# Kernel tuning notes

Hardware: AMD Instinct MI355X
Metric: run time of the kernel (lower is better)

## Reference

```python
import jax, jax.numpy as jnp
import numpy as np

B, H, L, D = 2, 16, 2048, 64

def _linear_feature_map(x, W):
    # x: [B,H,L,D], W: [H,D,E] -> relu(x @ W) per head, [B,H,L,E]
    return jax.nn.relu(jnp.einsum('bhld,hde->bhle', x, W))

def setup_inputs() -> dict:
    key = jax.random.key(0)
    ks = jax.random.split(key, 5)
    return {
        'query_states': jax.random.normal(ks[0], (B, H, L, D), dtype=jnp.float32),
        'key_states':   jax.random.normal(ks[1], (B, H, L, D), dtype=jnp.float32),
        'value_states': jax.random.normal(ks[2], (B, H, L, D), dtype=jnp.float32),
        'fm_q_weight':  jax.random.normal(ks[3], (H, D, D), dtype=jnp.float32),
        'fm_k_weight':  jax.random.normal(ks[4], (H, D, D), dtype=jnp.float32),
    }

def reference(query_states, key_states, value_states, fm_q_weight, fm_k_weight):
    # NOTE: source applies feature_map_k to queries and feature_map_q to keys (swapped); keep faithful.
    fq = _linear_feature_map(query_states, fm_k_weight)  # [B,H,L,D]
    fk = _linear_feature_map(key_states, fm_q_weight)    # [B,H,L,D]
    attn = jnp.einsum('bhld,bhkd->bhlk', fq, fk)         # [B,H,L,L]
    attn = jnp.tril(attn)                                # causal mask (attention_mask=None path)
    attn = attn / jnp.sum(attn, axis=-1, keepdims=True)  # row-normalize
    out = jnp.einsum('bhlk,bhkd->bhld', attn, value_states)
    return (out, attn)
```

## Files before the change

kernel.cpp:

```cpp
#include <hip/hip_runtime.h>
#include <hip/hip_bf16.h>

#define BB 2
#define HH 16
#define LL 2048
#define DD 64
constexpr int BH = BB * HH;
constexpr int NT = LL / 64;

typedef __attribute__((ext_vector_type(8))) short bf16x8;
typedef __attribute__((ext_vector_type(4))) float f32x4;

typedef unsigned short u16;
typedef unsigned int u32;

__device__ __forceinline__ u16 f2bf(float x) {
    __bf16 b = (__bf16)x;
    u16 u; __builtin_memcpy(&u, &b, 2);
    return u;
}
__device__ __forceinline__ float bf2f(u16 u) {
    union { u32 i; float f; } c; c.i = ((u32)u) << 16; return c.f;
}

__device__ __forceinline__ void gll16(const void* gptr, void* ldsptr) {
    __builtin_amdgcn_global_load_lds(
        (const u32 __attribute__((address_space(1)))*)gptr,
        (u32 __attribute__((address_space(3)))*)ldsptr, 16, 0, 0);
}

__device__ __forceinline__ bf16x8 ld_frag(const char* tile, int row, int kbyte) {
    return *(const bf16x8*)(tile + row * 128 + (kbyte ^ ((row & 7) << 4)));
}

template<bool TSUM>
__global__ __launch_bounds__(256) void fmap2_kernel(
    const float* __restrict__ x, const float* __restrict__ W,
    u16* __restrict__ ghi, float* __restrict__ tsum)
{
    __shared__ float sXT[64][64];
    __shared__ float sW[64][64];
    int bx = blockIdx.x;
    int bh = bx / NT, rb = bx % NT;
    int h = bh % HH;
    const float* xp = x + (size_t)bh * LL * DD + (size_t)rb * 64 * DD;
    const float* wp = W + (size_t)h * DD * DD;

    int tid = threadIdx.x;
    {
        int r = tid >> 2, c0 = (tid & 3) * 16;
        for (int u = 0; u < 16; u += 4) {
            float4 t = *(const float4*)(xp + r * DD + c0 + u);
            sXT[c0 + u + 0][r] = t.x; sXT[c0 + u + 1][r] = t.y;
            sXT[c0 + u + 2][r] = t.z; sXT[c0 + u + 3][r] = t.w;
            *(float4*)(&sW[r][c0 + u]) = *(const float4*)(wp + r * DD + c0 + u);
        }
    }
    __syncthreads();

    int ty = tid >> 4, tx = tid & 15;
    float acc[4][4] = {};
    #pragma unroll 4
    for (int d = 0; d < 64; ++d) {
        float4 a = *(const float4*)(&sXT[d][ty * 4]);
        float4 b = *(const float4*)(&sW[d][tx * 4]);
        float av[4] = {a.x, a.y, a.z, a.w};
        float bv[4] = {b.x, b.y, b.z, b.w};
        #pragma unroll
        for (int j = 0; j < 4; ++j)
            #pragma unroll
            for (int i = 0; i < 4; ++i)
                acc[j][i] = fmaf(av[j], bv[i], acc[j][i]);
    }

    char* hib = (char*)ghi + (size_t)bx * 8192;
    float colsum[4] = {0.f, 0.f, 0.f, 0.f};
    #pragma unroll
    for (int j = 0; j < 4; ++j) {
        int rr = ty * 4 + j;
        ushort4 hv;
        hv.x = f2bf(fmaxf(acc[j][0], 0.f));
        hv.y = f2bf(fmaxf(acc[j][1], 0.f));
        hv.z = f2bf(fmaxf(acc[j][2], 0.f));
        hv.w = f2bf(fmaxf(acc[j][3], 0.f));
        int off = rr * 128 + ((tx * 8) ^ ((rr & 7) << 4));
        *(ushort4*)(hib + off) = hv;
        if constexpr (TSUM) {
            colsum[0] += bf2f(hv.x); colsum[1] += bf2f(hv.y);
            colsum[2] += bf2f(hv.z); colsum[3] += bf2f(hv.w);
        }
    }

    if constexpr (TSUM) {
        __syncthreads();
        #pragma unroll
        for (int i = 0; i < 4; ++i)
            sXT[ty][tx * 4 + i] = colsum[i];
        __syncthreads();
        if (tid < 64) {
            float s = 0.f;
            #pragma unroll
            for (int y = 0; y < 16; ++y) s += sXT[y][tid];
            tsum[(size_t)bx * 64 + tid] = s;
        }
    }
}

__global__ __launch_bounds__(256) void vprep_kernel(
    const float* __restrict__ v, u16* __restrict__ vt)
{
    int bx = blockIdx.x;
    int bh = bx >> 5, ct = bx & 31;
    int t = threadIdx.x;
    int c0 = (t >> 4) * 4, e0 = (t & 15) * 4;
    const float* vp = v + ((size_t)bh * LL + (size_t)ct * 64) * DD;

    float ld[4][4];
    #pragma unroll
    for (int j = 0; j < 4; ++j) {
        float4 f = *(const float4*)(vp + (size_t)(c0 + j) * DD + e0);
        ld[j][0] = f.x; ld[j][1] = f.y; ld[j][2] = f.z; ld[j][3] = f.w;
    }
    char* base = (char*)vt + (size_t)bx * 8192;
    #pragma unroll
    for (int i = 0; i < 4; ++i) {
        int e = e0 + i;
        ushort4 wv;
        wv.x = f2bf(ld[0][i]); wv.y = f2bf(ld[1][i]);
        wv.z = f2bf(ld[2][i]); wv.w = f2bf(ld[3][i]);
        *(ushort4*)(base + e * 128 + ((c0 * 2) ^ ((e & 7) << 4))) = wv;
    }
}

__global__ __launch_bounds__(64) void tprefix_kernel(
    const float* __restrict__ tsum, float* __restrict__ pex)
{
    int bh = blockIdx.x, d = threadIdx.x;
    float run = 0.f;
    for (int t = 0; t < NT; ++t) {
        size_t i = ((size_t)bh * NT + t) * 64 + d;
        pex[i] = run;
        run += tsum[i];
    }
}

__global__ __launch_bounds__(256) void rowsum_kernel(
    const u16* __restrict__ khi, const u16* __restrict__ qhi,
    const float* __restrict__ pex, float* __restrict__ rinv)
{
    __shared__ float wsum[4][64];
    int bx = blockIdx.x;
    int bh = bx >> 5, t = bx & 31;
    int w = threadIdx.x >> 6, d = threadIdx.x & 63;
    const size_t tb = ((size_t)bh * NT + t) * 4096;

    float fkv[16];
    float s = 0.f;
    #pragma unroll
    for (int i = 0; i < 16; ++i) {
        int r = w * 16 + i;
        size_t idx = tb + r * 64 + (d ^ ((r & 7) << 3));
        fkv[i] = bf2f(khi[idx]);
        s += fkv[i];
    }
    wsum[w][d] = s;
    __syncthreads();

    float cs = pex[((size_t)bh * NT + t) * 64 + d];
    for (int w2 = 0; w2 < w; ++w2) cs += wsum[w2][d];

    #pragma unroll
    for (int i = 0; i < 16; ++i) {
        int r = w * 16 + i;
        size_t idx = tb + r * 64 + (d ^ ((r & 7) << 3));
        cs += fkv[i];
        float tt = bf2f(qhi[idx]) * cs;
        #pragma unroll
        for (int o = 1; o < 64; o <<= 1) tt += __shfl_xor(tt, o);
        if (d == 0) rinv[(size_t)bh * LL + t * 64 + r] = 1.0f / tt;
    }
}

__global__ __launch_bounds__(256, 4) void attn4_kernel(
    const u16* __restrict__ qhi, const u16* __restrict__ khi,
    const u16* __restrict__ vt, const float* __restrict__ rinvg,
    float* __restrict__ outO, float* __restrict__ outA)
{
    __shared__ __align__(16) char lds[40960];
    char* sS = lds + 32768;

    int bx = blockIdx.x;
    int bh = (bx & 7) * 4 + (bx >> 8);
    int jj = (bx >> 3) & 31;
    int rblk = (jj & 1) ? (jj >> 1) : (31 - (jj >> 1));
    int brow = rblk * 64;

    int tid = threadIdx.x;
    int w = tid >> 6, l = tid & 63;
    int l15 = l & 15, lq = l >> 4;
    int o = tid * 16, wb = w << 10;

    {
        const char* qT = (const char*)qhi + ((size_t)bh * NT + rblk) * 8192;
        gll16(qT + o,        lds + 16384 + wb);
        gll16(qT + o + 4096, lds + 16384 + wb + 4096);

        const char* kT = (const char*)khi + (size_t)bh * NT * 8192;
        const char* vT = (const char*)vt  + (size_t)bh * NT * 8192;
        gll16(kT + o,        lds + wb);
        gll16(kT + o + 4096, lds + wb + 4096);
        gll16(vT + o,        lds + 8192 + wb);
        gll16(vT + o + 4096, lds + 8192 + wb + 4096);
    }
    float ri = rinvg[(size_t)bh * LL + brow + w * 16 + l15];
    asm volatile("s_waitcnt vmcnt(0)" ::: "memory");
    __syncthreads();

    int qrow = w * 16 + l15;
    bf16x8 bq[2];
    #pragma unroll
    for (int ks = 0; ks < 2; ++ks)
        bq[ks] = ld_frag(lds + 16384, qrow, lq * 16 + ks * 64);
    __syncthreads();

    f32x4 acc2[4];
    #pragma unroll
    for (int eb = 0; eb < 4; ++eb) acc2[eb] = (f32x4){0.f, 0.f, 0.f, 0.f};

    for (int ct = 0; ct <= rblk; ++ct) {
        char* cur = lds + (ct & 1) * 16384;

        if (ct < rblk) {
            char* nxt = lds + ((ct + 1) & 1) * 16384;
            const char* kT = (const char*)khi + ((size_t)bh * NT + ct + 1) * 8192;
            const char* vT = (const char*)vt  + ((size_t)bh * NT + ct + 1) * 8192;
            gll16(kT + o,        nxt + wb);
            gll16(kT + o + 4096, nxt + wb + 4096);
            gll16(vT + o,        nxt + 8192 + wb);
            gll16(vT + o + 4096, nxt + 8192 + wb + 4096);
        }

        f32x4 sa[4];
        #pragma unroll
        for (int cb = 0; cb < 4; ++cb) sa[cb] = (f32x4){0.f, 0.f, 0.f, 0.f};
        #pragma unroll
        for (int ks = 0; ks < 2; ++ks) {
            #pragma unroll
            for (int cb = 0; cb < 4; ++cb) {
                bf16x8 ah = ld_frag(cur, cb * 16 + l15, lq * 16 + ks * 64);
                sa[cb] = __builtin_amdgcn_mfma_f32_16x16x32_bf16(ah, bq[ks], sa[cb], 0, 0, 0);
            }
        }

        bool diag = (ct == rblk);
        int srow = w * 16 + l15;
        #pragma unroll
        for (int cb = 0; cb < 4; ++cb) {
            if (diag) {
                #pragma unroll
                for (int rg = 0; rg < 4; ++rg)
                    if (cb * 16 + lq * 4 + rg > srow) sa[cb][rg] = 0.f;
            }
            sa[cb] *= ri;
            ushort4 pv;
            pv.x = f2bf(sa[cb][0]); pv.y = f2bf(sa[cb][1]);
            pv.z = f2bf(sa[cb][2]); pv.w = f2bf(sa[cb][3]);
            int soff = srow * 128 + ((cb * 32 + lq * 8) ^ ((srow & 7) << 4));
            *(ushort4*)(sS + soff) = pv;
        }

        asm volatile("s_waitcnt lgkmcnt(0)" ::: "memory");
        __builtin_amdgcn_sched_barrier(0);
        __builtin_amdgcn_s_barrier();
        __builtin_amdgcn_sched_barrier(0);

        {
            int bcol = ct * 64;
            float* atile = outA + ((size_t)bh * LL + brow) * LL + bcol;
            #pragma unroll
            for (int u = 0; u < 4; ++u) {
                int idx = tid + u * 256;
                int r = idx >> 4;
                int c = idx & 15;
                ushort4 pv = *(const ushort4*)(sS + r * 128 + ((c * 8) ^ ((r & 7) << 4)));
                f32x4 o4 = { bf2f(pv.x), bf2f(pv.y), bf2f(pv.z), bf2f(pv.w) };
                __builtin_nontemporal_store(o4, (f32x4*)(atile + (size_t)r * LL + c * 4));
            }
        }

        bf16x8 pf[2];
        #pragma unroll
        for (int ks = 0; ks < 2; ++ks)
            pf[ks] = ld_frag(sS, srow, lq * 16 + ks * 64);
        #pragma unroll
        for (int ks = 0; ks < 2; ++ks) {
            #pragma unroll
            for (int eb = 0; eb < 4; ++eb) {
                bf16x8 av = ld_frag(cur + 8192, eb * 16 + l15, lq * 16 + ks * 64);
                acc2[eb] = __builtin_amdgcn_mfma_f32_16x16x32_bf16(av, pf[ks], acc2[eb], 0, 0, 0);
            }
        }

        __syncthreads();
    }

    f32x4 z = {0.f, 0.f, 0.f, 0.f};
    for (int ct2 = rblk + 1; ct2 < NT; ++ct2) {
        int bcol = ct2 * 64;
        #pragma unroll
        for (int u = 0; u < 4; ++u) {
            int idx = tid + u * 256;
            int r = idx >> 4, c4 = idx & 15;
            __builtin_nontemporal_store(z,
                (f32x4*)(outA + ((size_t)bh * LL + brow + r) * LL + bcol + c4 * 4));
        }
    }

    float* oo = outO + ((size_t)bh * LL + brow + w * 16 + l15) * DD;
    #pragma unroll
    for (int eb = 0; eb < 4; ++eb) {
        float4 o4 = { acc2[eb][0], acc2[eb][1], acc2[eb][2], acc2[eb][3] };
        *(float4*)(oo + eb * 16 + lq * 4) = o4;
    }
}

extern "C" void kernel_launch(void* const* d_in, const int* in_sizes, int n_in,
                              void* d_out, int out_size, void* d_ws, size_t ws_size,
                              hipStream_t stream)
{
    (void)in_sizes; (void)n_in; (void)out_size; (void)ws_size;
    const float* q  = (const float*)d_in[0];
    const float* k  = (const float*)d_in[1];
    const float* v  = (const float*)d_in[2];
    const float* Wq = (const float*)d_in[3];
    const float* Wk = (const float*)d_in[4];

    float* out  = (float*)d_out;
    float* attn = out + (size_t)BB * HH * LL * DD;

    const size_t TILE_HW = (size_t)BH * NT * 4096;
    u16* QHI = (u16*)d_ws;
    u16* KHI = QHI + TILE_HW;
    u16* VT  = KHI + TILE_HW;
    float* RINV = (float*)(VT + TILE_HW);
    float* TSUM = RINV + (size_t)BH * LL;
    float* PEX  = TSUM + (size_t)BH * NT * 64;

    fmap2_kernel<false><<<BH * NT, 256, 0, stream>>>(q, Wk, QHI, nullptr);
    fmap2_kernel<true><<<BH * NT, 256, 0, stream>>>(k, Wq, KHI, TSUM);
    vprep_kernel<<<BH * NT, 256, 0, stream>>>(v, VT);
    tprefix_kernel<<<BH, 64, 0, stream>>>(TSUM, PEX);
    rowsum_kernel<<<BH * NT, 256, 0, stream>>>(KHI, QHI, PEX, RINV);
    attn4_kernel<<<BH * NT, 256, 0, stream>>>(QHI, KHI, VT, RINV, out, attn);
}
```

Measured before the change: 173.0 us.

## Fuse V prep and tile prefix into other kernels; pair row blocks per attention block

Measured after the change: 175.1 us. No clear change (+1.2%).

```diff
diff --git a/kernel.cpp b/kernel.cpp
--- a/kernel.cpp
+++ b/kernel.cpp
@@ -33,10 +33,11 @@
     return *(const bf16x8*)(tile + row * 128 + (kbyte ^ ((row & 7) << 4)));
 }
 
-template<bool TSUM>
+template<bool TSUM, bool VPREP>
 __global__ __launch_bounds__(256) void fmap2_kernel(
     const float* __restrict__ x, const float* __restrict__ W,
-    u16* __restrict__ ghi, float* __restrict__ tsum)
+    u16* __restrict__ ghi, float* __restrict__ tsum,
+    const float* __restrict__ v, u16* __restrict__ vt)
 {
     __shared__ float sXT[64][64];
     __shared__ float sW[64][64];
@@ -104,49 +105,31 @@
             tsum[(size_t)bx * 64 + tid] = s;
         }
     }
-}
-
-__global__ __launch_bounds__(256) void vprep_kernel(
-    const float* __restrict__ v, u16* __restrict__ vt)
-{
-    int bx = blockIdx.x;
-    int bh = bx >> 5, ct = bx & 31;
-    int t = threadIdx.x;
-    int c0 = (t >> 4) * 4, e0 = (t & 15) * 4;
-    const float* vp = v + ((size_t)bh * LL + (size_t)ct * 64) * DD;
-
-    float ld[4][4];
-    #pragma unroll
-    for (int j = 0; j < 4; ++j) {
-        float4 f = *(const float4*)(vp + (size_t)(c0 + j) * DD + e0);
-        ld[j][0] = f.x; ld[j][1] = f.y; ld[j][2] = f.z; ld[j][3] = f.w;
-    }
-    char* base = (char*)vt + (size_t)bx * 8192;
-    #pragma unroll
-    for (int i = 0; i < 4; ++i) {
-        int e = e0 + i;
-        ushort4 wv;
-        wv.x = f2bf(ld[0][i]); wv.y = f2bf(ld[1][i]);
-        wv.z = f2bf(ld[2][i]); wv.w = f2bf(ld[3][i]);
-        *(ushort4*)(base + e * 128 + ((c0 * 2) ^ ((e & 7) << 4))) = wv;
-    }
-}
-
-__global__ __launch_bounds__(64) void tprefix_kernel(
-    const float* __restrict__ tsum, float* __restrict__ pex)
-{
-    int bh = blockIdx.x, d = threadIdx.x;
-    float run = 0.f;
-    for (int t = 0; t < NT; ++t) {
-        size_t i = ((size_t)bh * NT + t) * 64 + d;
-        pex[i] = run;
-        run += tsum[i];
+
+    if constexpr (VPREP) {
+        int c0 = (tid >> 4) * 4, e0 = (tid & 15) * 4;
+        const float* vp = v + ((size_t)bh * LL + (size_t)rb * 64) * DD;
+        float ld[4][4];
+        #pragma unroll
+        for (int j = 0; j < 4; ++j) {
+            float4 f = *(const float4*)(vp + (size_t)(c0 + j) * DD + e0);
+            ld[j][0] = f.x; ld[j][1] = f.y; ld[j][2] = f.z; ld[j][3] = f.w;
+        }
+        char* base = (char*)vt + (size_t)bx * 8192;
+        #pragma unroll
+        for (int i = 0; i < 4; ++i) {
+            int e = e0 + i;
+            ushort4 wv;
+            wv.x = f2bf(ld[0][i]); wv.y = f2bf(ld[1][i]);
+            wv.z = f2bf(ld[2][i]); wv.w = f2bf(ld[3][i]);
+            *(ushort4*)(base + e * 128 + ((c0 * 2) ^ ((e & 7) << 4))) = wv;
+        }
     }
 }
 
 __global__ __launch_bounds__(256) void rowsum_kernel(
     const u16* __restrict__ khi, const u16* __restrict__ qhi,
-    const float* __restrict__ pex, float* __restrict__ rinv)
+    const float* __restrict__ tsum, float* __restrict__ rinv)
 {
     __shared__ float wsum[4][64];
     int bx = blockIdx.x;
@@ -166,7 +149,9 @@
     wsum[w][d] = s;
     __syncthreads();
 
-    float cs = pex[((size_t)bh * NT + t) * 64 + d];
+    float cs = 0.f;
+    for (int t2 = 0; t2 < t; ++t2)
+        cs += tsum[((size_t)bh * NT + t2) * 64 + d];
     for (int w2 = 0; w2 < w; ++w2) cs += wsum[w2][d];
 
     #pragma unroll
@@ -181,7 +166,7 @@
     }
 }
 
-__global__ __launch_bounds__(256, 4) void attn4_kernel(
+__global__ __launch_bounds__(256, 4) void attn5_kernel(
     const u16* __restrict__ qhi, const u16* __restrict__ khi,
     const u16* __restrict__ vt, const float* __restrict__ rinvg,
     float* __restrict__ outO, float* __restrict__ outA)
@@ -190,137 +175,140 @@
     char* sS = lds + 32768;
 
     int bx = blockIdx.x;
-    int bh = (bx & 7) * 4 + (bx >> 8);
-    int jj = (bx >> 3) & 31;
-    int rblk = (jj & 1) ? (jj >> 1) : (31 - (jj >> 1));
-    int brow = rblk * 64;
+    int bh = bx & 31;
+    int p = bx >> 5;
 
     int tid = threadIdx.x;
     int w = tid >> 6, l = tid & 63;
     int l15 = l & 15, lq = l >> 4;
     int o = tid * 16, wb = w << 10;
 
-    {
-        const char* qT = (const char*)qhi + ((size_t)bh * NT + rblk) * 8192;
-        gll16(qT + o,        lds + 16384 + wb);
-        gll16(qT + o + 4096, lds + 16384 + wb + 4096);
-
-        const char* kT = (const char*)khi + (size_t)bh * NT * 8192;
-        const char* vT = (const char*)vt  + (size_t)bh * NT * 8192;
-        gll16(kT + o,        lds + wb);
-        gll16(kT + o + 4096, lds + wb + 4096);
-        gll16(vT + o,        lds + 8192 + wb);
-        gll16(vT + o + 4096, lds + 8192 + wb + 4096);
-    }
-    float ri = rinvg[(size_t)bh * LL + brow + w * 16 + l15];
-    asm volatile("s_waitcnt vmcnt(0)" ::: "memory");
-    __syncthreads();
-
-    int qrow = w * 16 + l15;
-    bf16x8 bq[2];
-    #pragma unroll
-    for (int ks = 0; ks < 2; ++ks)
-        bq[ks] = ld_frag(lds + 16384, qrow, lq * 16 + ks * 64);
-    __syncthreads();
-
-    f32x4 acc2[4];
-    #pragma unroll
-    for (int eb = 0; eb < 4; ++eb) acc2[eb] = (f32x4){0.f, 0.f, 0.f, 0.f};
-
-    for (int ct = 0; ct <= rblk; ++ct) {
-        char* cur = lds + (ct & 1) * 16384;
-
-        if (ct < rblk) {
-            char* nxt = lds + ((ct + 1) & 1) * 16384;
-            const char* kT = (const char*)khi + ((size_t)bh * NT + ct + 1) * 8192;
-            const char* vT = (const char*)vt  + ((size_t)bh * NT + ct + 1) * 8192;
-            gll16(kT + o,        nxt + wb);
-            gll16(kT + o + 4096, nxt + wb + 4096);
-            gll16(vT + o,        nxt + 8192 + wb);
-            gll16(vT + o + 4096, nxt + 8192 + wb + 4096);
-        }
-
-        f32x4 sa[4];
-        #pragma unroll
-        for (int cb = 0; cb < 4; ++cb) sa[cb] = (f32x4){0.f, 0.f, 0.f, 0.f};
-        #pragma unroll
-        for (int ks = 0; ks < 2; ++ks) {
+    for (int half = 0; half < 2; ++half) {
+        int rblk = half ? (31 - p) : p;
+        int brow = rblk * 64;
+
+        {
+            const char* qT = (const char*)qhi + ((size_t)bh * NT + rblk) * 8192;
+            gll16(qT + o,        lds + 16384 + wb);
+            gll16(qT + o + 4096, lds + 16384 + wb + 4096);
+
+            const char* kT = (const char*)khi + (size_t)bh * NT * 8192;
+            const char* vT = (const char*)vt  + (size_t)bh * NT * 8192;
+            gll16(kT + o,        lds + wb);
+            gll16(kT + o + 4096, lds + wb + 4096);
+            gll16(vT + o,        lds + 8192 + wb);
+            gll16(vT + o + 4096, lds + 8192 + wb + 4096);
+        }
+        float ri = rinvg[(size_t)bh * LL + brow + w * 16 + l15];
+        asm volatile("s_waitcnt vmcnt(0)" ::: "memory");
+        __syncthreads();
+
+        int qrow = w * 16 + l15;
+        bf16x8 bq[2];
+        #pragma unroll
+        for (int ks = 0; ks < 2; ++ks)
+            bq[ks] = ld_frag(lds + 16384, qrow, lq * 16 + ks * 64);
+        __syncthreads();
+
+        f32x4 acc2[4];
+        #pragma unroll
+        for (int eb = 0; eb < 4; ++eb) acc2[eb] = (f32x4){0.f, 0.f, 0.f, 0.f};
+
+        for (int ct = 0; ct <= rblk; ++ct) {
+            char* cur = lds + (ct & 1) * 16384;
+
+            if (ct < rblk) {
+                char* nxt = lds + ((ct + 1) & 1) * 16384;
+                const char* kT = (const char*)khi + ((size_t)bh * NT + ct + 1) * 8192;
+                const char* vT = (const char*)vt  + ((size_t)bh * NT + ct + 1) * 8192;
+                gll16(kT + o,        nxt + wb);
+                gll16(kT + o + 4096, nxt + wb + 4096);
+                gll16(vT + o,        nxt + 8192 + wb);
+                gll16(vT + o + 4096, nxt + 8192 + wb + 4096);
+            }
+
+            f32x4 sa[4];
+            #pragma unroll
+            for (int cb = 0; cb < 4; ++cb) sa[cb] = (f32x4){0.f, 0.f, 0.f, 0.f};
+            #pragma unroll
+            for (int ks = 0; ks < 2; ++ks) {
+                #pragma unroll
+                for (int cb = 0; cb < 4; ++cb) {
+                    bf16x8 ah = ld_frag(cur, cb * 16 + l15, lq * 16 + ks * 64);
+                    sa[cb] = __builtin_amdgcn_mfma_f32_16x16x32_bf16(ah, bq[ks], sa[cb], 0, 0, 0);
+                }
+            }
+
+            bool diag = (ct == rblk);
+            int srow = w * 16 + l15;
             #pragma unroll
             for (int cb = 0; cb < 4; ++cb) {
-                bf16x8 ah = ld_frag(cur, cb * 16 + l15, lq * 16 + ks * 64);
-                sa[cb] = __builtin_amdgcn_mfma_f32_16x16x32_bf16(ah, bq[ks], sa[cb], 0, 0, 0);
-            }
-        }
-
-        bool diag = (ct == rblk);
-        int srow = w * 16 + l15;
-        #pragma unroll
-        for (int cb = 0; cb < 4; ++cb) {
-            if (diag) {
+                if (diag) {
+                    #pragma unroll
+                    for (int rg = 0; rg < 4; ++rg)
+                        if (cb * 16 + lq * 4 + rg > srow) sa[cb][rg] = 0.f;
+                }
+                sa[cb] *= ri;
+                ushort4 pv;
+                pv.x = f2bf(sa[cb][0]); pv.y = f2bf(sa[cb][1]);
+                pv.z = f2bf(sa[cb][2]); pv.w = f2bf(sa[cb][3]);
+                int soff = srow * 128 + ((cb * 32 + lq * 8) ^ ((srow & 7) << 4));
+                *(ushort4*)(sS + soff) = pv;
+            }
+
+            asm volatile("s_waitcnt lgkmcnt(0)" ::: "memory");
+            __builtin_amdgcn_sched_barrier(0);
+            __builtin_amdgcn_s_barrier();
+            __builtin_amdgcn_sched_barrier(0);
+
+            {
+                int bcol = ct * 64;
+                float* atile = outA + ((size_t)bh * LL + brow) * LL + bcol;
                 #pragma unroll
-                for (int rg = 0; rg < 4; ++rg)
-                    if (cb * 16 + lq * 4 + rg > srow) sa[cb][rg] = 0.f;
-            }
-            sa[cb] *= ri;
-            ushort4 pv;
-            pv.x = f2bf(sa[cb][0]); pv.y = f2bf(sa[cb][1]);
-            pv.z = f2bf(sa[cb][2]); pv.w = f2bf(sa[cb][3]);
-            int soff = srow * 128 + ((cb * 32 + lq * 8) ^ ((srow & 7) << 4));
-            *(ushort4*)(sS + soff) = pv;
-        }
-
-        asm volatile("s_waitcnt lgkmcnt(0)" ::: "memory");
-        __builtin_amdgcn_sched_barrier(0);
-        __builtin_amdgcn_s_barrier();
-        __builtin_amdgcn_sched_barrier(0);
-
-        {
-            int bcol = ct * 64;
-            float* atile = outA + ((size_t)bh * LL + brow) * LL + bcol;
+                for (int u = 0; u < 4; ++u) {
+                    int idx = tid + u * 256;
+                    int r = idx >> 4;
+                    int c = idx & 15;
+                    ushort4 pv = *(const ushort4*)(sS + r * 128 + ((c * 8) ^ ((r & 7) << 4)));
+                    f32x4 o4 = { bf2f(pv.x), bf2f(pv.y), bf2f(pv.z), bf2f(pv.w) };
+                    __builtin_nontemporal_store(o4, (f32x4*)(atile + (size_t)r * LL + c * 4));
+                }
+            }
+
+            bf16x8 pf[2];
+            #pragma unroll
+            for (int ks = 0; ks < 2; ++ks)
+                pf[ks] = ld_frag(sS, srow, lq * 16 + ks * 64);
+            #pragma unroll
+            for (int ks = 0; ks < 2; ++ks) {
+                #pragma unroll
+                for (int eb = 0; eb < 4; ++eb) {
+                    bf16x8 av = ld_frag(cur + 8192, eb * 16 + l15, lq * 16 + ks * 64);
+                    acc2[eb] = __builtin_amdgcn_mfma_f32_16x16x32_bf16(av, pf[ks], acc2[eb], 0, 0, 0);
+                }
+            }
+
+            __syncthreads();
+        }
+
+        f32x4 z = {0.f, 0.f, 0.f, 0.f};
+        for (int ct2 = rblk + 1; ct2 < NT; ++ct2) {
+            int bcol = ct2 * 64;
             #pragma unroll
             for (int u = 0; u < 4; ++u) {
                 int idx = tid + u * 256;
-                int r = idx >> 4;
-                int c = idx & 15;
-                ushort4 pv = *(const ushort4*)(sS + r * 128 + ((c * 8) ^ ((r & 7) << 4)));
-                f32x4 o4 = { bf2f(pv.x), bf2f(pv.y), bf2f(pv.z), bf2f(pv.w) };
-                __builtin_nontemporal_store(o4, (f32x4*)(atile + (size_t)r * LL + c * 4));
-            }
-        }
-
-        bf16x8 pf[2];
-        #pragma unroll
-        for (int ks = 0; ks < 2; ++ks)
-            pf[ks] = ld_frag(sS, srow, lq * 16 + ks * 64);
-        #pragma unroll
-        for (int ks = 0; ks < 2; ++ks) {
-            #pragma unroll
-            for (int eb = 0; eb < 4; ++eb) {
-                bf16x8 av = ld_frag(cur + 8192, eb * 16 + l15, lq * 16 + ks * 64);
-                acc2[eb] = __builtin_amdgcn_mfma_f32_16x16x32_bf16(av, pf[ks], acc2[eb], 0, 0, 0);
-            }
-        }
-
-        __syncthreads();
-    }
-
-    f32x4 z = {0.f, 0.f, 0.f, 0.f};
-    for (int ct2 = rblk + 1; ct2 < NT; ++ct2) {
-        int bcol = ct2 * 64;
-        #pragma unroll
-        for (int u = 0; u < 4; ++u) {
-            int idx = tid + u * 256;
-            int r = idx >> 4, c4 = idx & 15;
-            __builtin_nontemporal_store(z,
-                (f32x4*)(outA + ((size_t)bh * LL + brow + r) * LL + bcol + c4 * 4));
-        }
-    }
-
-    float* oo = outO + ((size_t)bh * LL + brow + w * 16 + l15) * DD;
-    #pragma unroll
-    for (int eb = 0; eb < 4; ++eb) {
-        float4 o4 = { acc2[eb][0], acc2[eb][1], acc2[eb][2], acc2[eb][3] };
-        *(float4*)(oo + eb * 16 + lq * 4) = o4;
+                int r = idx >> 4, c4 = idx & 15;
+                __builtin_nontemporal_store(z,
+                    (f32x4*)(outA + ((size_t)bh * LL + brow + r) * LL + bcol + c4 * 4));
+            }
+        }
+
+        float* oo = outO + ((size_t)bh * LL + brow + w * 16 + l15) * DD;
+        #pragma unroll
+        for (int eb = 0; eb < 4; ++eb) {
+            float4 o4 = { acc2[eb][0], acc2[eb][1], acc2[eb][2], acc2[eb][3] };
+            *(float4*)(oo + eb * 16 + lq * 4) = o4;
+        }
     }
 }
 
@@ -344,12 +332,9 @@
     u16* VT  = KHI + TILE_HW;
     float* RINV = (float*)(VT + TILE_HW);
     float* TSUM = RINV + (size_t)BH * LL;
-    float* PEX  = TSUM + (size_t)BH * NT * 64;
-
-    fmap2_kernel<false><<<BH * NT, 256, 0, stream>>>(q, Wk, QHI, nullptr);
-    fmap2_kernel<true><<<BH * NT, 256, 0, stream>>>(k, Wq, KHI, TSUM);
-    vprep_kernel<<<BH * NT, 256, 0, stream>>>(v, VT);
-    tprefix_kernel<<<BH, 64, 0, stream>>>(TSUM, PEX);
-    rowsum_kernel<<<BH * NT, 256, 0, stream>>>(KHI, QHI, PEX, RINV);
-    attn4_kernel<<<BH * NT, 256, 0, stream>>>(QHI, KHI, VT, RINV, out, attn);
-}
+
+    fmap2_kernel<false, true><<<BH * NT, 256, 0, stream>>>(q, Wk, QHI, nullptr, v, VT);
+    fmap2_kernel<true, false><<<BH * NT, 256, 0, stream>>>(k, Wq, KHI, TSUM, nullptr, nullptr);
+    rowsum_kernel<<<BH * NT, 256, 0, stream>>>(KHI, QHI, TSUM, RINV);
+    attn5_kernel<<<BH * 16, 256, 0, stream>>>(QHI, KHI, VT, RINV, out, attn);
+}
```
